# Performance work log

Hardware: AMD Instinct MI355X
Metric: run time of the kernel (lower is better)

The kernel has to match this reference:

```python
import jax, jax.numpy as jnp
import numpy as np
from jax import lax

B, T, V, C = 16, 128, 137, 3
IOC = [(64, 64), (64, 128), (128, 256)]  # (in_c, out_c), all strides 1
OUT0 = 64
K = 9
PAD = (K - 1) // 2
NUM_CLASS = 226
DELTA = 0.5
BN_EPS = 1e-5


def setup_inputs() -> dict:
    key = jax.random.key(0)
    ks = jax.random.split(key, 16)
    inp = {"X": jax.random.normal(ks[0], (B, T, V, C), dtype=jnp.float32)}
    # data_bn params over V*C channels
    inp["bn_gamma"] = jnp.ones((V * C,), jnp.float32)
    inp["bn_beta"] = jnp.zeros((V * C,), jnp.float32)
    # gtcn0 conv
    inp["w0"] = jax.random.normal(ks[1], (OUT0, C, K, 1), jnp.float32) * np.sqrt(2.0 / (C * K))
    inp["b0"] = jnp.zeros((OUT0,), jnp.float32)
    for i, (ic, oc) in enumerate(IOC):
        inp[f"w{i+1}"] = jax.random.normal(ks[2 + i], (oc, ic, K, 1), jnp.float32) * np.sqrt(2.0 / (ic * K))
        inp[f"b{i+1}"] = jnp.zeros((oc,), jnp.float32)
    inp["fc_w"] = jax.random.normal(ks[8], (NUM_CLASS, IOC[-1][1]), jnp.float32) * 0.02
    inp["fc_b"] = jnp.zeros((NUM_CLASS,), jnp.float32)
    return inp


def _adj(X):
    # Gaussian-kernel affinity per (batch, frame): exp(-||xi-xj|| / (2*delta^2)).
    # Original builds this on CPU with scipy.cdist inside torch.tensor (detached),
    # so we stop gradients through it.
    Xs = lax.stop_gradient(X)  # [B,T,V,C]
    diff = Xs[:, :, :, None, :] - Xs[:, :, None, :, :]  # [B,T,V,V,C]
    dist = jnp.sqrt(jnp.sum(diff * diff, axis=-1))       # euclidean, like cdist
    return jnp.exp(-dist / (2.0 * DELTA ** 2))            # [B,T,V,V]


def _conv(x, w, b):
    # Conv2d kernel (K,1), padding ((K-1)//2, 0), stride (1,1)
    y = lax.conv_general_dilated(x, w, window_strides=(1, 1),
                                 padding=[(PAD, PAD), (0, 0)],
                                 dimension_numbers=("NCHW", "OIHW", "NCHW"))
    return y + b[None, :, None, None]


def reference(X, bn_gamma, bn_beta, w0, b0, w1, b1, w2, b2, w3, b3, fc_w, fc_b):
    A = _adj(X)  # [B,T,V,V]
    # data_bn: BatchNorm1d over V*C channels (training-mode batch stats)
    Xr = jnp.einsum("btvc->bvct", X).reshape(B, V * C, T)
    mean = Xr.mean(axis=(0, 2), keepdims=True)
    var = Xr.var(axis=(0, 2), keepdims=True)
    Xn = (Xr - mean) * jax.lax.rsqrt(var + BN_EPS)
    Xn = Xn * bn_gamma[None, :, None] + bn_beta[None, :, None]
    x = jnp.einsum("bvct->bctv", Xn.reshape(B, V, C, T))  # [B,C,T,V]
    x = _conv(x, w0, b0)
    for w, b in ((w1, b1), (w2, b2), (w3, b3)):
        ax = jnp.einsum("bctv,btvw->bctw", x, A)  # graph matmul X @ A per (b,t)
        x = jax.nn.relu(_conv(ax, w, b))
    x = x.mean(axis=(2, 3))  # [B, C_out]
    return x @ fc_w.T + fc_b  # [B, num_class]
```

## Files before the change

### kernel.cpp

```cpp
#include <hip/hip_runtime.h>
#include <hip/hip_bf16.h>
#include <math.h>

#define BB 16
#define TT 128
#define VV 137
#define CCH 3
#define NN (VV*TT)
#define NCLS 226
#define APITCH 23040

typedef __attribute__((ext_vector_type(8))) short bf16x8;
typedef __attribute__((ext_vector_type(4))) float f32x4;

__device__ __forceinline__ unsigned short f2bf(float x) {
  __hip_bfloat16 h = __float2bfloat16(x);
  return *reinterpret_cast<unsigned short*>(&h);
}

__device__ __forceinline__ void gld_lds16(const unsigned short* src, unsigned short* ldst) {
  __builtin_amdgcn_global_load_lds(
      (const __attribute__((address_space(1))) void*)src,
      (__attribute__((address_space(3))) void*)ldst, 16, 0, 0);
}

__global__ void bn_stats_kernel(const float* __restrict__ X,
                                const float* __restrict__ gamma,
                                const float* __restrict__ beta,
                                float* __restrict__ scale,
                                float* __restrict__ shift) {
  const int ch = blockIdx.x;
  const int v = ch / CCH, c = ch % CCH;
  const int tid = threadIdx.x;
  float s = 0.f, q = 0.f;
  for (int idx = tid; idx < BB*TT; idx += 256) {
    float x = X[(idx*VV + v)*CCH + c];
    s += x; q += x*x;
  }
  #pragma unroll
  for (int off = 32; off > 0; off >>= 1) {
    s += __shfl_down(s, off, 64);
    q += __shfl_down(q, off, 64);
  }
  __shared__ float ls[4], lq[4];
  const int wid = tid >> 6, lane = tid & 63;
  if (lane == 0) { ls[wid] = s; lq[wid] = q; }
  __syncthreads();
  if (tid == 0) {
    float S = ls[0]+ls[1]+ls[2]+ls[3];
    float Q = lq[0]+lq[1]+lq[2]+lq[3];
    const float inv_n = 1.f / (BB*TT);
    float mean = S * inv_n;
    float var = Q * inv_n - mean*mean;
    float sc = gamma[ch] * rsqrtf(var + 1e-5f);
    scale[ch] = sc;
    shift[ch] = beta[ch] - mean * sc;
  }
}

__global__ void bn_apply_v(const float* __restrict__ X,
                           const float* __restrict__ scale,
                           const float* __restrict__ shift,
                           unsigned short* __restrict__ xn) {
  const int o = blockIdx.x*256 + threadIdx.x;
  if (o >= BB*NN*CCH) return;
  const int c = o % CCH;
  const int n = (o / CCH) % NN;
  const int b = o / (CCH*NN);
  const int v = n >> 7, t = n & 127;
  const int ch = v*CCH + c;
  float val = X[((b*TT + t)*VV + v)*CCH + c] * scale[ch] + shift[ch];
  xn[o] = f2bf(val);
}

__global__ void wtrans_kernel(const float* __restrict__ w, unsigned short* __restrict__ wT,
                              int OC, int IC) {
  const int o = blockIdx.x*256 + threadIdx.x;
  if (o >= OC*IC*9) return;
  const int ic = o % IC;
  const int oc = (o / IC) % OC;
  const int kk = o / (IC*OC);
  wT[o] = f2bf(w[(oc*IC + ic)*9 + kk]);
}

__global__ void w0trans_kernel(const float* __restrict__ w0, unsigned short* __restrict__ w0T) {
  const int o = blockIdx.x*256 + threadIdx.x;
  if (o >= 64*32) return;
  const int k = o % 32, oc = o / 32;
  const int kk = k / 3, ic = k % 3;
  w0T[o] = (k < 27) ? f2bf(w0[(oc*3 + ic)*9 + kk]) : (unsigned short)0;
}

__global__ void zero_kernel(float* __restrict__ p, int n) {
  const int i = blockIdx.x*256 + threadIdx.x;
  if (i < n) p[i] = 0.f;
}

__global__ __launch_bounds__(256)
void adj_v(const float* __restrict__ X, unsigned short* __restrict__ A) {
  __shared__ float Xs[3][144];
  const int b = blockIdx.x / TT, t = blockIdx.x % TT;
  const int tid = threadIdx.x;
  for (int i = tid; i < 3*VV; i += 256) {
    const int c = i / VV, v = i % VV;
    Xs[c][v] = X[((b*TT + t)*VV + v)*CCH + c];
  }
  __syncthreads();
  unsigned short* Ab = A + (size_t)blockIdx.x * APITCH;
  for (int e = tid; e < 144*160; e += 256) {
    const int w = e / 160, v = e % 160;
    unsigned short val = 0;
    if (w < VV && v < VV) {
      const float d0 = Xs[0][v]-Xs[0][w];
      const float d1 = Xs[1][v]-Xs[1][w];
      const float d2 = Xs[2][v]-Xs[2][w];
      val = f2bf(__expf(-2.f * sqrtf(d0*d0 + d1*d1 + d2*d2)));
    }
    Ab[e] = val;
  }
}

__global__ __launch_bounds__(256)
void conv0_v(const unsigned short* __restrict__ xn,
             const unsigned short* __restrict__ w0T,
             const float* __restrict__ bias,
             unsigned short* __restrict__ outp) {
  __shared__ unsigned short im_s[128*40];
  __shared__ unsigned short w_s[64*40];
  __shared__ unsigned short ob[128*72];
  const int tid = threadIdx.x;
  const int v0 = blockIdx.x % 137;
  const int b  = blockIdx.x / 137;
  const int wave = tid >> 6, lane = tid & 63, quad = lane >> 4, l15 = lane & 15;
  const int mh = wave * 32;

  {
    const int row = tid >> 2, cg = tid & 3;
    *(uint4*)&w_s[row*40 + cg*8] = *(const uint4*)(w0T + row*32 + cg*8);
  }
  for (int e = tid; e < 128*32; e += 256) {
    const int t = e >> 5, k = e & 31;
    unsigned short val = 0;
    if (k < 27) {
      const int kk = k / 3, ic = k % 3;
      const int tp = t + kk - 4;
      if (tp >= 0 && tp < TT)
        val = xn[((size_t)b*NN + (size_t)v0*TT + tp)*3 + ic];
    }
    im_s[t*40 + k] = val;
  }
  __syncthreads();

  f32x4 acc[2][4];
  #pragma unroll
  for (int mt = 0; mt < 2; ++mt)
    #pragma unroll
    for (int ct = 0; ct < 4; ++ct) acc[mt][ct] = (f32x4){0.f,0.f,0.f,0.f};

  bf16x8 af[2], bfr[4];
  #pragma unroll
  for (int mt = 0; mt < 2; ++mt)
    af[mt] = *(const bf16x8*)&im_s[(mh + mt*16 + l15)*40 + quad*8];
  #pragma unroll
  for (int ct = 0; ct < 4; ++ct)
    bfr[ct] = *(const bf16x8*)&w_s[(ct*16 + l15)*40 + quad*8];
  #pragma unroll
  for (int mt = 0; mt < 2; ++mt)
    #pragma unroll
    for (int ct = 0; ct < 4; ++ct)
      acc[mt][ct] = __builtin_amdgcn_mfma_f32_16x16x32_bf16(af[mt], bfr[ct], acc[mt][ct], 0, 0, 0);

  #pragma unroll
  for (int mt = 0; mt < 2; ++mt) {
    const int tb = mh + mt*16 + quad*4;
    #pragma unroll
    for (int ct = 0; ct < 4; ++ct) {
      const int oc = ct*16 + l15;
      const float bv = bias[oc];
      #pragma unroll
      for (int r = 0; r < 4; ++r)
        ob[(tb + r)*72 + oc] = f2bf(acc[mt][ct][r] + bv);
    }
  }
  __syncthreads();
  for (int rr = 0; rr < 4; ++rr) {
    const int idx = rr*256 + tid;
    const int t = idx >> 3, cg = idx & 7;
    uint4 val = *(const uint4*)&ob[t*72 + cg*8];
    *(uint4*)(outp + ((size_t)b*NN + (size_t)v0*TT + t)*64 + cg*8) = val;
  }
}

template<int IC, int OCB, int NCT, int RELU, int FUSE>
__global__ __launch_bounds__(256)
void conv_v2(const unsigned short* __restrict__ in,
             const unsigned short* __restrict__ wT,
             const float* __restrict__ bias,
             unsigned short* __restrict__ outp,
             float* __restrict__ mout,
             const unsigned short* __restrict__ zbuf,
             int OCtot, int nocb) {
  constexpr int NWIN = 136*IC/512;
  constexpr int TWIN = 2*NWIN;
  constexpr int WWIN = OCB*IC/512;
  constexpr int GPR  = IC/8;
  constexpr int RPW  = 512/IC;
  constexpr int INSZ = 2*136*IC;
  constexpr int WSZ  = OCB*IC;
  constexpr int OCP  = OCB + 8;
  constexpr int OBSZ = FUSE ? 0 : 256*OCP;
  constexpr int TOT  = (INSZ + 2*WSZ > OBSZ) ? (INSZ + 2*WSZ) : OBSZ;
  __shared__ unsigned short sh[TOT];
  unsigned short* in_s = sh;
  unsigned short* ob = sh;

  const int tid = threadIdx.x;
  const int wave = tid >> 6, lane = tid & 63, quad = lane >> 4, l15 = lane & 15;
  const int pair = blockIdx.x % 69;
  const int ocby = (blockIdx.x / 69) % nocb;
  const int b    = blockIdx.x / (69*nocb);
  const int v0 = pair*2;
  const int ocb0 = ocby * OCB;
  const int vr = wave >> 1;
  const int mhl = (wave & 1) * 64;
  const bool vok = (v0 + vr) < VV;

  const int lrow = lane / GPR;
  const int lg   = lane % GPR;

  #pragma unroll
  for (int wi = 0; wi < (TWIN+3)/4; ++wi) {
    const int W = wave + 4*wi;
    if (W < TWIN) {
      const int vrW = W / NWIN;
      const int rl = (W % NWIN)*RPW + lrow;
      const int t = rl - 4;
      const int sg = lg ^ (rl & 7);
      const unsigned short* src = (t >= 0 && t < TT && (v0+vrW) < VV)
          ? in + ((size_t)b*NN + (size_t)(v0+vrW)*TT + t)*IC + (sg<<3)
          : zbuf + lane*8;
      gld_lds16(src, in_s + W*512);
    }
  }
  auto stage_w = [&](int kk, int buf) {
    unsigned short* wb = sh + INSZ + buf*WSZ;
    #pragma unroll
    for (int wi = 0; wi < WWIN/4; ++wi) {
      const int W = wave + 4*wi;
      const int row = W*RPW + lrow;
      const int sg = lg ^ (row & 7);
      gld_lds16(wT + ((size_t)kk*OCtot + ocb0 + row)*IC + (sg<<3), wb + W*512);
    }
  };
  stage_w(0, 0);
  __syncthreads();

  f32x4 acc[4][NCT];
  #pragma unroll
  for (int mt = 0; mt < 4; ++mt)
    #pragma unroll
    for (int ct = 0; ct < NCT; ++ct) acc[mt][ct] = (f32x4){0.f,0.f,0.f,0.f};

  for (int kk = 0; kk < 9; ++kk) {
    if (kk < 8) stage_w(kk+1, (kk+1) & 1);
    const unsigned short* wb = sh + INSZ + (kk & 1)*WSZ;
    #pragma unroll
    for (int ks = 0; ks < IC/32; ++ks) {
      const int G = ks*4 + quad;
      bf16x8 af[4], bfr[NCT];
      #pragma unroll
      for (int mt = 0; mt < 4; ++mt) {
        const int row = mhl + mt*16 + l15 + kk;
        af[mt] = *(const bf16x8*)&in_s[vr*(136*IC) + row*IC + ((G ^ (row & 7)) << 3)];
      }
      #pragma unroll
      for (int ct = 0; ct < NCT; ++ct) {
        const int row = ct*16 + l15;
        bfr[ct] = *(const bf16x8*)&wb[row*IC + ((G ^ (row & 7)) << 3)];
      }
      #pragma unroll
      for (int mt = 0; mt < 4; ++mt)
        #pragma unroll
        for (int ct = 0; ct < NCT; ++ct)
          acc[mt][ct] = __builtin_amdgcn_mfma_f32_16x16x32_bf16(af[mt], bfr[ct], acc[mt][ct], 0, 0, 0);
    }
    __syncthreads();
  }

  if (FUSE) {
    if (vok) {
      #pragma unroll
      for (int ct = 0; ct < NCT; ++ct) {
        const int oc = ocb0 + ct*16 + l15;
        const float bv = bias[oc];
        float s = 0.f;
        #pragma unroll
        for (int mt = 0; mt < 4; ++mt)
          #pragma unroll
          for (int r = 0; r < 4; ++r) {
            float x = acc[mt][ct][r] + bv;
            if (RELU) x = fmaxf(x, 0.f);
            s += x;
          }
        s += __shfl_down(s, 32, 64);
        s += __shfl_down(s, 16, 64);
        if (lane < 16) atomicAdd(&mout[(size_t)b*OCtot + oc], s * (1.f / NN));
      }
    }
  } else {
    #pragma unroll
    for (int mt = 0; mt < 4; ++mt) {
      const int ro = vr*128 + mhl + mt*16 + quad*4;
      #pragma unroll
      for (int ct = 0; ct < NCT; ++ct) {
        const int oc = ct*16 + l15;
        const float bv = bias[oc];
        #pragma unroll
        for (int r = 0; r < 4; ++r) {
          float x = acc[mt][ct][r] + bv;
          if (RELU) x = fmaxf(x, 0.f);
          ob[(ro + r)*OCP + oc] = f2bf(x);
        }
      }
    }
    __syncthreads();
    constexpr int GPO = OCB/8;
    #pragma unroll
    for (int it = 0; it < 256*GPO/256; ++it) {
      const int task = it*256 + tid;
      const int ro = task / GPO, g = task % GPO;
      const int vrow = v0 + (ro >> 7);
      if (vrow < VV) {
        uint4 val = *(const uint4*)&ob[ro*OCP + g*8];
        *(uint4*)(outp + ((size_t)b*NN + (size_t)vrow*TT + (ro & 127))*OCB + g*8) = val;
      }
    }
  }
}

__global__ __launch_bounds__(256)
void gmm_v2(const unsigned short* __restrict__ A,
            const unsigned short* __restrict__ act,
            unsigned short* __restrict__ outp,
            int Cfull) {
  __shared__ unsigned short xt[64*192];
  __shared__ unsigned short ob[144*72];
  const int bt = blockIdx.x;
  const int b = bt / TT, t = bt % TT;
  const int ch = blockIdx.y;
  const int tid = threadIdx.x;
  const int wave = tid >> 6, lane = tid & 63, quad = lane >> 4, l15 = lane & 15;

  #pragma unroll
  for (int it = 0; it < 5; ++it) {
    const int task = it*256 + tid;
    const int v = task >> 3, g = task & 7;
    uint4 val = {0u,0u,0u,0u};
    if (v < VV)
      val = *(const uint4*)(act + ((size_t)b*NN + (size_t)v*TT + t)*Cfull + ch*64 + g*8);
    const unsigned short* pv = (const unsigned short*)&val;
    const int vg = v >> 3, vrm = v & 7;
    #pragma unroll
    for (int j = 0; j < 8; ++j) {
      const int c = g*8 + j;
      const int slot = ((vg ^ (c & 7) ^ ((c >> 3) & 7)) << 3) | vrm;
      xt[c*192 + slot] = pv[j];
    }
  }
  __syncthreads();

  const unsigned short* Abt = A + (size_t)bt * APITCH;
  f32x4 acc[9];
  #pragma unroll
  for (int ct = 0; ct < 9; ++ct) acc[ct] = (f32x4){0.f,0.f,0.f,0.f};

  const int m = wave*16 + l15;
  #pragma unroll
  for (int ks = 0; ks < 5; ++ks) {
    const int G = ks*4 + quad;
    const int slot = (G ^ (m & 7) ^ ((m >> 3) & 7)) << 3;
    const bf16x8 af = *(const bf16x8*)&xt[m*192 + slot];
    #pragma unroll
    for (int ct = 0; ct < 9; ++ct) {
      const bf16x8 bfv = *(const bf16x8*)(Abt + (ct*16 + l15)*160 + ks*32 + quad*8);
      acc[ct] = __builtin_amdgcn_mfma_f32_16x16x32_bf16(af, bfv, acc[ct], 0, 0, 0);
    }
  }

  #pragma unroll
  for (int ct = 0; ct < 9; ++ct) {
    const int w = ct*16 + l15;
    #pragma unroll
    for (int r = 0; r < 4; ++r) {
      const int c = wave*16 + quad*4 + r;
      ob[w*72 + c] = f2bf(acc[ct][r]);
    }
  }
  __syncthreads();
  {
    const int wl = tid >> 3, cg = tid & 7;
    #pragma unroll
    for (int rr = 0; rr < 5; ++rr) {
      const int w = rr*32 + wl;
      if (w < VV) {
        uint4 val = *(const uint4*)&ob[w*72 + cg*8];
        *(uint4*)(outp + ((size_t)b*NN + (size_t)w*TT + t)*Cfull + ch*64 + cg*8) = val;
      }
    }
  }
}

__global__ void fc_kernel(const float* __restrict__ mean,
                          const float* __restrict__ fcw,
                          const float* __restrict__ fcb,
                          float* __restrict__ out) {
  const int b = blockIdx.x;
  __shared__ float ms[256];
  const int tid = threadIdx.x;
  ms[tid] = mean[b*256 + tid];
  __syncthreads();
  if (tid < NCLS) {
    float acc = fcb[tid];
    for (int c = 0; c < 256; ++c) acc = fmaf(ms[c], fcw[tid*256 + c], acc);
    out[b*NCLS + tid] = acc;
  }
}

extern "C" void kernel_launch(void* const* d_in, const int* in_sizes, int n_in,
                              void* d_out, int out_size, void* d_ws, size_t ws_size,
                              hipStream_t stream) {
  const float* X    = (const float*)d_in[0];
  const float* bn_g = (const float*)d_in[1];
  const float* bn_b = (const float*)d_in[2];
  const float* w0   = (const float*)d_in[3];
  const float* cb0  = (const float*)d_in[4];
  const float* w1   = (const float*)d_in[5];
  const float* cb1  = (const float*)d_in[6];
  const float* w2   = (const float*)d_in[7];
  const float* cb2  = (const float*)d_in[8];
  const float* w3   = (const float*)d_in[9];
  const float* cb3  = (const float*)d_in[10];
  const float* fcw  = (const float*)d_in[11];
  const float* fcb  = (const float*)d_in[12];
  float* out = (float*)d_out;

  unsigned char* W = (unsigned char*)d_ws;
  size_t off = 0;
  auto alloc = [&](size_t bytes) -> void* {
    void* p = W + off;
    off += (bytes + 255) & ~(size_t)255;
    return p;
  };
  float* meanb  = (float*)alloc(BB*256*4);
  float* zbuf_f = (float*)alloc(2048);
  float* scale  = (float*)alloc(512*4);
  float* shiftb = (float*)alloc(512*4);
  unsigned short* w0T = (unsigned short*)alloc(64*32*2);
  unsigned short* wT1 = (unsigned short*)alloc((size_t)9*64*64*2);
  unsigned short* wT2 = (unsigned short*)alloc((size_t)9*128*64*2);
  unsigned short* wT3 = (unsigned short*)alloc((size_t)9*256*128*2);
  unsigned short* xn  = (unsigned short*)alloc((size_t)BB*NN*3*2);
  const size_t fixedB = off;
  const size_t perB = 2*((size_t)NN*128*2 + 256) + ((size_t)TT*APITCH*2 + 256);

  int g = 1;
  if (ws_size > fixedB + perB) {
    size_t gg = (ws_size - fixedB) / perB;
    g = (gg >= BB) ? BB : (int)gg;
  }
  unsigned short* P  = (unsigned short*)alloc((size_t)g*NN*128*2);
  unsigned short* Q  = (unsigned short*)alloc((size_t)g*NN*128*2);
  unsigned short* Ab = (unsigned short*)alloc((size_t)g*TT*APITCH*2);
  const unsigned short* zbuf = (const unsigned short*)zbuf_f;

  bn_stats_kernel<<<411, 256, 0, stream>>>(X, bn_g, bn_b, scale, shiftb);
  bn_apply_v<<<(BB*NN*3 + 255)/256, 256, 0, stream>>>(X, scale, shiftb, xn);
  w0trans_kernel<<<(64*32 + 255)/256, 256, 0, stream>>>(w0, w0T);
  wtrans_kernel<<<(9*64*64   + 255)/256, 256, 0, stream>>>(w1, wT1, 64, 64);
  wtrans_kernel<<<(9*128*64  + 255)/256, 256, 0, stream>>>(w2, wT2, 128, 64);
  wtrans_kernel<<<(9*256*128 + 255)/256, 256, 0, stream>>>(w3, wT3, 256, 128);
  zero_kernel<<<((BB*256 + 512) + 255)/256, 256, 0, stream>>>(meanb, BB*256 + 512);

  for (int b0 = 0; b0 < BB; b0 += g) {
    const int gb = (BB - b0 < g) ? (BB - b0) : g;
    const float* Xg = X + (size_t)b0 * TT * VV * CCH;
    const unsigned short* xng = xn + (size_t)b0 * NN * 3;
    float* mg = meanb + (size_t)b0 * 256;

    adj_v<<<gb*TT, 256, 0, stream>>>(Xg, Ab);
    conv0_v<<<137*gb, 256, 0, stream>>>(xng, w0T, cb0, P);
    gmm_v2<<<dim3(gb*TT, 1), 256, 0, stream>>>(Ab, P, Q, 64);
    conv_v2<64,64,4,1,0><<<69*gb, 256, 0, stream>>>(Q, wT1, cb1, P, nullptr, zbuf, 64, 1);
    gmm_v2<<<dim3(gb*TT, 1), 256, 0, stream>>>(Ab, P, Q, 64);
    conv_v2<64,128,8,1,0><<<69*gb, 256, 0, stream>>>(Q, wT2, cb2, P, nullptr, zbuf, 128, 1);
    gmm_v2<<<dim3(gb*TT, 2), 256, 0, stream>>>(Ab, P, Q, 128);
    conv_v2<128,128,8,1,1><<<69*2*gb, 256, 0, stream>>>(Q, wT3, cb3, nullptr, mg, zbuf, 256, 2);
  }

  fc_kernel<<<BB, 256, 0, stream>>>(meanb, fcw, fcb, out);
}
```

Before: 612.1 us.

## Add single-vertex-row conv variant with output-channel wave split and optional single weight buffer

Result: faster. 547.2 us (-10.6%).

```diff
diff --git a/kernel.cpp b/kernel.cpp
--- a/kernel.cpp
+++ b/kernel.cpp
@@ -191,39 +191,43 @@
   }
 }
 
-template<int IC, int OCB, int NCT, int RELU, int FUSE>
+template<int IC, int OCB, int VROWS, int WDBUF, int RELU, int FUSE>
 __global__ __launch_bounds__(256)
-void conv_v2(const unsigned short* __restrict__ in,
+void conv_v3(const unsigned short* __restrict__ in,
              const unsigned short* __restrict__ wT,
              const float* __restrict__ bias,
              unsigned short* __restrict__ outp,
              float* __restrict__ mout,
              const unsigned short* __restrict__ zbuf,
              int OCtot, int nocb) {
+  constexpr int NCT  = (VROWS == 2) ? OCB/16 : OCB/32;
   constexpr int NWIN = 136*IC/512;
-  constexpr int TWIN = 2*NWIN;
+  constexpr int TWIN = VROWS*NWIN;
   constexpr int WWIN = OCB*IC/512;
   constexpr int GPR  = IC/8;
   constexpr int RPW  = 512/IC;
-  constexpr int INSZ = 2*136*IC;
+  constexpr int INSZ = VROWS*136*IC;
   constexpr int WSZ  = OCB*IC;
+  constexpr int NWB  = WDBUF ? 2 : 1;
   constexpr int OCP  = OCB + 8;
-  constexpr int OBSZ = FUSE ? 0 : 256*OCP;
-  constexpr int TOT  = (INSZ + 2*WSZ > OBSZ) ? (INSZ + 2*WSZ) : OBSZ;
+  constexpr int OBSZ = FUSE ? 0 : VROWS*128*OCP;
+  constexpr int TOT  = (INSZ + NWB*WSZ > OBSZ) ? (INSZ + NWB*WSZ) : OBSZ;
   __shared__ unsigned short sh[TOT];
   unsigned short* in_s = sh;
   unsigned short* ob = sh;
 
   const int tid = threadIdx.x;
   const int wave = tid >> 6, lane = tid & 63, quad = lane >> 4, l15 = lane & 15;
-  const int pair = blockIdx.x % 69;
-  const int ocby = (blockIdx.x / 69) % nocb;
-  const int b    = blockIdx.x / (69*nocb);
-  const int v0 = pair*2;
+  const int nv = (VROWS == 2) ? 69 : 137;
+  const int grp  = blockIdx.x % nv;
+  const int ocby = (blockIdx.x / nv) % nocb;
+  const int b    = blockIdx.x / (nv*nocb);
+  const int v0 = grp * VROWS;
   const int ocb0 = ocby * OCB;
-  const int vr = wave >> 1;
-  const int mhl = (wave & 1) * 64;
-  const bool vok = (v0 + vr) < VV;
+  const int vr  = (VROWS == 2) ? (wave >> 1) : 0;
+  const int mhl = (VROWS == 2) ? ((wave & 1) * 64) : ((wave >> 1) * 64);
+  const int chb = (VROWS == 2) ? 0 : ((wave & 1) * (OCB >> 1));
+  const bool vok = (VROWS == 1) || ((v0 + vr) < VV);
 
   const int lrow = lane / GPR;
   const int lg   = lane % GPR;
@@ -252,8 +256,6 @@
       gld_lds16(wT + ((size_t)kk*OCtot + ocb0 + row)*IC + (sg<<3), wb + W*512);
     }
   };
-  stage_w(0, 0);
-  __syncthreads();
 
   f32x4 acc[4][NCT];
   #pragma unroll
@@ -261,9 +263,8 @@
     #pragma unroll
     for (int ct = 0; ct < NCT; ++ct) acc[mt][ct] = (f32x4){0.f,0.f,0.f,0.f};
 
-  for (int kk = 0; kk < 9; ++kk) {
-    if (kk < 8) stage_w(kk+1, (kk+1) & 1);
-    const unsigned short* wb = sh + INSZ + (kk & 1)*WSZ;
+  auto compute_kk = [&](int kk, int buf) {
+    const unsigned short* wb = sh + INSZ + buf*WSZ;
     #pragma unroll
     for (int ks = 0; ks < IC/32; ++ks) {
       const int G = ks*4 + quad;
@@ -275,7 +276,7 @@
       }
       #pragma unroll
       for (int ct = 0; ct < NCT; ++ct) {
-        const int row = ct*16 + l15;
+        const int row = chb + ct*16 + l15;
         bfr[ct] = *(const bf16x8*)&wb[row*IC + ((G ^ (row & 7)) << 3)];
       }
       #pragma unroll
@@ -284,14 +285,30 @@
         for (int ct = 0; ct < NCT; ++ct)
           acc[mt][ct] = __builtin_amdgcn_mfma_f32_16x16x32_bf16(af[mt], bfr[ct], acc[mt][ct], 0, 0, 0);
     }
+  };
+
+  if (WDBUF) {
+    stage_w(0, 0);
     __syncthreads();
+    for (int kk = 0; kk < 9; ++kk) {
+      if (kk < 8) stage_w(kk+1, (kk+1) & 1);
+      compute_kk(kk, kk & 1);
+      __syncthreads();
+    }
+  } else {
+    for (int kk = 0; kk < 9; ++kk) {
+      stage_w(kk, 0);
+      __syncthreads();
+      compute_kk(kk, 0);
+      __syncthreads();
+    }
   }
 
   if (FUSE) {
     if (vok) {
       #pragma unroll
       for (int ct = 0; ct < NCT; ++ct) {
-        const int oc = ocb0 + ct*16 + l15;
+        const int oc = ocb0 + chb + ct*16 + l15;
         const float bv = bias[oc];
         float s = 0.f;
         #pragma unroll
@@ -313,8 +330,8 @@
       const int ro = vr*128 + mhl + mt*16 + quad*4;
       #pragma unroll
       for (int ct = 0; ct < NCT; ++ct) {
-        const int oc = ct*16 + l15;
-        const float bv = bias[oc];
+        const int oc = chb + ct*16 + l15;
+        const float bv = bias[ocb0 + oc];
         #pragma unroll
         for (int r = 0; r < 4; ++r) {
           float x = acc[mt][ct][r] + bv;
@@ -326,7 +343,7 @@
     __syncthreads();
     constexpr int GPO = OCB/8;
     #pragma unroll
-    for (int it = 0; it < 256*GPO/256; ++it) {
+    for (int it = 0; it < VROWS*128*GPO/256; ++it) {
       const int task = it*256 + tid;
       const int ro = task / GPO, g = task % GPO;
       const int vrow = v0 + (ro >> 7);
@@ -490,11 +507,11 @@
     adj_v<<<gb*TT, 256, 0, stream>>>(Xg, Ab);
     conv0_v<<<137*gb, 256, 0, stream>>>(xng, w0T, cb0, P);
     gmm_v2<<<dim3(gb*TT, 1), 256, 0, stream>>>(Ab, P, Q, 64);
-    conv_v2<64,64,4,1,0><<<69*gb, 256, 0, stream>>>(Q, wT1, cb1, P, nullptr, zbuf, 64, 1);
+    conv_v3<64,64,2,1,1,0><<<69*gb, 256, 0, stream>>>(Q, wT1, cb1, P, nullptr, zbuf, 64, 1);
     gmm_v2<<<dim3(gb*TT, 1), 256, 0, stream>>>(Ab, P, Q, 64);
-    conv_v2<64,128,8,1,0><<<69*gb, 256, 0, stream>>>(Q, wT2, cb2, P, nullptr, zbuf, 128, 1);
+    conv_v3<64,128,1,1,1,0><<<137*gb, 256, 0, stream>>>(Q, wT2, cb2, P, nullptr, zbuf, 128, 1);
     gmm_v2<<<dim3(gb*TT, 2), 256, 0, stream>>>(Ab, P, Q, 128);
-    conv_v2<128,128,8,1,1><<<69*2*gb, 256, 0, stream>>>(Q, wT3, cb3, nullptr, mg, zbuf, 256, 2);
+    conv_v3<128,128,1,0,1,1><<<137*2*gb, 256, 0, stream>>>(Q, wT3, cb3, nullptr, mg, zbuf, 256, 2);
   }
 
   fc_kernel<<<BB, 256, 0, stream>>>(meanb, fcw, fcb, out);
```
